# Performance work log

Hardware: AMD Instinct MI355X
Metric: run time of the kernel (lower is better)

The kernel has to match this reference:

```python
import jax, jax.numpy as jnp
import numpy as np

K = 20
EPS = 1e-5


def _lrelu(x):
    return jax.nn.leaky_relu(x, 0.2)


def _bn(x, axes):
    # Training-mode batch norm with default affine (gamma=1, beta=0)
    m = jnp.mean(x, axis=axes, keepdims=True)
    v = jnp.var(x, axis=axes, keepdims=True)
    return (x - m) / jnp.sqrt(v + EPS)


def _get_graph_feature(x, k):
    # x: [B, C, N] -> [B, 2C, N, k]
    xx = jnp.sum(x * x, axis=1)                     # [B, N]
    inner = jnp.einsum('bcn,bcm->bnm', x, x)        # [B, N, N]
    pd = 2.0 * inner - xx[:, :, None] - xx[:, None, :]  # -||xi-xj||^2
    idx = jax.lax.top_k(pd, k)[1]                   # [B, N, k] nearest neighbors
    xt = jnp.transpose(x, (0, 2, 1))                # [B, N, C]
    feat = jax.vmap(lambda a, i: a[i])(xt, idx)     # [B, N, k, C] gathered neighbors
    center = jnp.broadcast_to(xt[:, :, None, :], feat.shape)
    out = jnp.concatenate([feat - center, center], axis=-1)  # [B, N, k, 2C]
    return jnp.transpose(out, (0, 3, 1, 2))


def _pconv(w, x):
    # 1x1 Conv2d, no bias: [O,C] x [B,C,N,k] -> [B,O,N,k]
    return jnp.einsum('oc,bcnk->bonk', w, x)


def _transform_net(x0, t_w1, t_w2, t_w3, t_fc1_w, t_fc2_w, t_fc2_b, t_fc3_w, t_fc3_b):
    h = _lrelu(_bn(_pconv(t_w1, x0), (0, 2, 3)))    # [B,64,N,k]
    h = _lrelu(_bn(_pconv(t_w2, h), (0, 2, 3)))     # [B,128,N,k]
    h = jnp.max(h, axis=-1)                         # [B,128,N]
    h = jnp.einsum('oc,bcn->bon', t_w3, h)          # [B,1024,N]
    h = _lrelu(_bn(h, (0, 2)))
    h = jnp.max(h, axis=-1)                         # [B,1024]
    h = _lrelu(_bn(h @ t_fc1_w.T, (0,)))            # [B,512]
    h = _lrelu(_bn(h @ t_fc2_w.T + t_fc2_b, (0,)))  # [B,256]
    h = h @ t_fc3_w.T + t_fc3_b                     # [B,9]
    h = h + jnp.eye(3, dtype=h.dtype).reshape(1, 9)
    return h.reshape(-1, 3, 3)


def setup_inputs() -> dict:
    key = jax.random.key(0)
    ks = jax.random.split(key, 16)
    s = 0.05
    B, N = 8, 1024
    return {
        'x': jax.random.normal(ks[0], (B, 3, N), jnp.float32),
        't_w1': jax.random.normal(ks[1], (64, 6), jnp.float32) * s,
        't_w2': jax.random.normal(ks[2], (128, 64), jnp.float32) * s,
        't_w3': jax.random.normal(ks[3], (1024, 128), jnp.float32) * s,
        't_fc1_w': jax.random.normal(ks[4], (512, 1024), jnp.float32) * s,
        't_fc2_w': jax.random.normal(ks[5], (256, 512), jnp.float32) * s,
        't_fc2_b': jnp.zeros((256,), jnp.float32),
        't_fc3_w': jax.random.normal(ks[6], (9, 256), jnp.float32) * s,
        't_fc3_b': jnp.zeros((9,), jnp.float32),
        'w1': jax.random.normal(ks[7], (64, 6), jnp.float32) * s,
        'w2': jax.random.normal(ks[8], (64, 128), jnp.float32) * s,
        'w3': jax.random.normal(ks[9], (128, 128), jnp.float32) * s,
        'w4': jax.random.normal(ks[10], (256, 256), jnp.float32) * s,
        'w6': jax.random.normal(ks[11], (1024, 512), jnp.float32) * s,
    }


def reference(x, t_w1, t_w2, t_w3, t_fc1_w, t_fc2_w, t_fc2_b, t_fc3_w, t_fc3_b,
              w1, w2, w3, w4, w6):
    # Input transform
    x0 = _get_graph_feature(x, K)                   # [B,6,N,k]
    T = _transform_net(x0, t_w1, t_w2, t_w3, t_fc1_w, t_fc2_w, t_fc2_b,
                       t_fc3_w, t_fc3_b)            # [B,3,3]
    x = jnp.einsum('bij,bjn->bin', T, x)            # [B,3,N]

    # EdgeConv stack
    g = _get_graph_feature(x, K)
    x1 = jnp.max(_lrelu(_bn(_pconv(w1, g), (0, 2, 3))), axis=-1)   # [B,64,N]
    g = _get_graph_feature(x1, K)
    x2 = jnp.max(_lrelu(_bn(_pconv(w2, g), (0, 2, 3))), axis=-1)   # [B,64,N]
    g = _get_graph_feature(x2, K)
    x3 = jnp.max(_lrelu(_bn(_pconv(w3, g), (0, 2, 3))), axis=-1)   # [B,128,N]
    g = _get_graph_feature(x3, K)
    x4 = jnp.max(_lrelu(_bn(_pconv(w4, g), (0, 2, 3))), axis=-1)   # [B,256,N]

    x_cat = jnp.concatenate([x1, x2, x3, x4], axis=1)              # [B,512,N]
    x_fea = x_cat  # adapt_layer_off: source unavailable, identity passthrough

    h = jnp.einsum('oc,bcn->bon', w6, x_fea)                       # [B,1024,N]
    h = _lrelu(_bn(h, (0, 2)))
    return jnp.max(h, axis=-1)                                     # [B,1024]
```

## Files before the change

kernel.cpp:

```cpp
#include <hip/hip_runtime.h>
#include <math.h>

#define BN_ 8
#define NN 1024
#define KK 20
#define EPSBN 1e-5f
#define FXSCALE 1048576.0f

typedef unsigned long long u64;

__device__ __forceinline__ float lrelu(float x){ return x > 0.f ? x : 0.2f*x; }

__device__ __forceinline__ unsigned fmap(float x){
  unsigned u = __float_as_uint(x);
  return (u & 0x80000000u) ? ~u : (u | 0x80000000u);
}
__device__ __forceinline__ float funmap(unsigned m){
  unsigned u = (m & 0x80000000u) ? (m & 0x7FFFFFFFu) : ~m;
  return __uint_as_float(u);
}

__device__ __forceinline__ void statadd(u64* SP, int O, int ch, int o, float s, float s2){
  atomicAdd(&SP[(size_t)ch*2*O + o],     (u64)(long long)llrintf(s  * FXSCALE));
  atomicAdd(&SP[(size_t)ch*2*O + O + o], (u64)(long long)llrintf(s2 * FXSCALE));
}

__global__ void k_transq(const float* __restrict__ src, long bs, int C,
                         float* __restrict__ xt, float* __restrict__ xx)
{
  int g = blockIdx.x*256 + threadIdx.x;
  if (g >= BN_*NN) return;
  int b = g >> 10, n = g & 1023;
  const float* s = src + (long)b*bs + n;
  float* d = xt + (long)g*C;
  float ss = 0.f;
  for (int c = 0; c < C; ++c){ float v = s[(long)c*NN]; d[c] = v; ss += v*v; }
  xx[g] = ss;
}

__global__ __launch_bounds__(256) void k_knn(
    const float* __restrict__ X, long bsX,
    const float* __restrict__ XT, const float* __restrict__ XX,
    int* __restrict__ IDX, int C)
{
  extern __shared__ float sm[];
  int tid = threadIdx.x;
  int wave = tid >> 6, lane = tid & 63;
  int row0 = blockIdx.x << 2;
  int b = row0 >> 10;
  int i0 = row0 & 1023;
  for (int t = tid; t < 4*C; t += 256){
    int rr = t / C, cc = t - rr*C;
    sm[t] = XT[((long)(b<<10) + i0 + rr)*C + cc];
  }
  __syncthreads();
  const float* xb = X + (long)b*bsX;
  float acc[16];
  #pragma unroll
  for (int q=0;q<16;q++) acc[q]=0.f;
  const float* xi = sm + wave*C;
  for (int c = 0; c < C; ++c){
    const float* xr = xb + (long)c*NN + lane;
    float xiv = xi[c];
    #pragma unroll
    for (int q=0;q<16;q++) acc[q] = fmaf(xiv, xr[q*64], acc[q]);
  }
  const float* xxb = XX + (b<<10);
  float xxj[16];
  #pragma unroll
  for (int q=0;q<16;q++) xxj[q] = xxb[q*64 + lane];
  int row = i0 + wave;
  float xxi = xxb[row];
  #pragma unroll
  for (int q=0;q<16;q++) acc[q] = 2.f*acc[q] - xxi - xxj[q];

  int outbase = ((b<<10) + row)*KK;
  for (int round=0; round<KK; ++round){
    float bv = -INFINITY; int bq = 0;
    #pragma unroll
    for (int q=0;q<16;q++){ float v = acc[q]; if (v > bv){ bv = v; bq = q; } }
    int bj = bq*64 + lane;
    #pragma unroll
    for (int off=32; off>0; off>>=1){
      float ov = __shfl_xor(bv, off);
      int oj = __shfl_xor(bj, off);
      if (ov > bv || (ov == bv && oj < bj)){ bv = ov; bj = oj; }
    }
    bool mine = (lane == (bj & 63));
    int mq = bj >> 6;
    #pragma unroll
    for (int q=0;q<16;q++)
      acc[q] = (mine && q == mq) ? -INFINITY : acc[q];
    if (lane == 0) IDX[outbase + round] = bj;
  }
}

__global__ void k_edgeconv3(const float* __restrict__ XT, const int* __restrict__ IDX,
                            const float* __restrict__ W, float* __restrict__ YMT,
                            u64* __restrict__ SP)
{
  __shared__ float nb[KK*3];
  __shared__ float ctr[3];
  __shared__ int is[KK];
  const int C = 3, O = 64;
  int tid = threadIdx.x;
  int bn = blockIdx.x;
  int b = bn >> 10;
  if (tid < KK) is[tid] = IDX[bn*KK + tid];
  __syncthreads();
  if (tid < 60){ int k = tid/3, c = tid - k*3; nb[tid] = XT[((long)(b<<10)+is[k])*C + c]; }
  if (tid < 3) ctr[tid] = XT[(long)bn*C + tid];
  __syncthreads();
  int o = tid;
  const float* wp = W + (long)o*2*C;
  float yc = 0.f;
  #pragma unroll
  for (int c = 0; c < 3; ++c) yc = fmaf(wp[C+c] - wp[c], ctr[c], yc);
  float acc[KK];
  #pragma unroll
  for (int k=0;k<KK;k++) acc[k] = yc;
  #pragma unroll
  for (int c = 0; c < 3; ++c){
    float wf = wp[c];
    #pragma unroll
    for (int k=0;k<KK;k++) acc[k] = fmaf(wf, nb[k*3+c], acc[k]);
  }
  float mx = -INFINITY, s = 0.f, s2 = 0.f;
  #pragma unroll
  for (int k=0;k<KK;k++){ float v = acc[k]; mx = fmaxf(mx, v); s += v; s2 = fmaf(v,v,s2); }
  YMT[(long)bn*O + o] = mx;
  statadd(SP, O, bn & 63, o, s, s2);
}

template<int C, int O>
__global__ __launch_bounds__(256) void k_gemm_ab(
    const float* __restrict__ XT, const float* __restrict__ WP,
    float* __restrict__ AB)
{
  constexpr int P = 16;
  constexpr int TWO = 2*O;
  constexpr int CO = (TWO + 255)/256;
  __shared__ __align__(16) float Xs[P][C];
  int tid = threadIdx.x;
  long bn0 = (long)blockIdx.x * P;
  for (int t = tid; t < P*C; t += 256) (&Xs[0][0])[t] = XT[bn0*C + t];
  __syncthreads();
  float acc[CO][P];
  #pragma unroll
  for (int j=0;j<CO;j++)
    #pragma unroll
    for (int r=0;r<P;r++) acc[j][r] = 0.f;
  for (int c4 = 0; c4 < C/4; ++c4){
    float4 w[CO];
    #pragma unroll
    for (int j=0;j<CO;j++){
      int o = tid + j*256;
      if (o < TWO) w[j] = *(const float4*)(WP + ((size_t)c4*TWO + o)*4);
    }
    #pragma unroll
    for (int r=0;r<P;r++){
      float4 xv = *(const float4*)(&Xs[r][c4*4]);
      #pragma unroll
      for (int j=0;j<CO;j++){
        acc[j][r] = fmaf(w[j].x, xv.x, acc[j][r]);
        acc[j][r] = fmaf(w[j].y, xv.y, acc[j][r]);
        acc[j][r] = fmaf(w[j].z, xv.z, acc[j][r]);
        acc[j][r] = fmaf(w[j].w, xv.w, acc[j][r]);
      }
    }
  }
  #pragma unroll
  for (int j=0;j<CO;j++){
    int o = tid + j*256;
    if (o < TWO)
      for (int r=0;r<P;r++) AB[(bn0 + r)*TWO + o] = acc[j][r];
  }
}

template<int O, int P>
__global__ __launch_bounds__(256) void k_egather(
    const float* __restrict__ AB, const int* __restrict__ IDX,
    float* __restrict__ YMT, u64* __restrict__ SP)
{
  constexpr int TWO = 2*O;
  constexpr int S = 256/O;
  constexpr int PS = P/S;
  __shared__ int is[P][KK];
  int tid = threadIdx.x;
  long bn0 = (long)blockIdx.x * P;
  long b10 = (bn0 >> 10) << 10;
  for (int t = tid; t < P*KK; t += 256) (&is[0][0])[t] = IDX[bn0*KK + t];
  __syncthreads();
  int strand = tid / O;
  int o = tid - strand*O;
  float s = 0.f, s2 = 0.f;
  #pragma unroll
  for (int ps = 0; ps < PS; ++ps){
    int p = strand*PS + ps;
    long bn = bn0 + p;
    float bv = AB[bn*TWO + O + o];
    float mx = -INFINITY;
    #pragma unroll
    for (int k = 0; k < KK; ++k){
      long row = b10 + is[p][k];
      float v = AB[row*TWO + o] + bv;
      mx = fmaxf(mx, v);
      s += v; s2 = fmaf(v,v,s2);
    }
    YMT[bn*O + o] = mx;
  }
  int ch = ((int)blockIdx.x * S + strand) & 63;
  statadd(SP, O, ch, o, s, s2);
}

__global__ void k_bnfin(const u64* __restrict__ SP, float* __restrict__ MV, int O, float cnt)
{
  int o = blockIdx.x*blockDim.x + threadIdx.x;
  if (o >= O) return;
  long long S = 0, S2 = 0;
  for (int ch = 0; ch < 64; ++ch){
    S  += (long long)SP[(size_t)ch*2*O + o];
    S2 += (long long)SP[(size_t)ch*2*O + O + o];
  }
  double m = (double)S / ((double)FXSCALE * (double)cnt);
  double ms2 = (double)S2 / ((double)FXSCALE * (double)cnt);
  double var = ms2 - m*m;
  MV[o] = (float)m;
  MV[O + o] = (float)(1.0 / sqrt(var + (double)EPSBN));
}

__global__ __launch_bounds__(64) void k_tconv2(
    const float* __restrict__ XT, const int* __restrict__ IDX,
    const float* __restrict__ W1, const float* __restrict__ MV1,
    const float* __restrict__ W2T, float* __restrict__ M2T, u64* __restrict__ SP)
{
  __shared__ float nb[KK*3];
  __shared__ float ctr[3];
  __shared__ __align__(16) float h1t[64*KK];
  __shared__ int is[KK];
  int tid = threadIdx.x;
  int bn = blockIdx.x;
  int b = bn >> 10;
  if (tid < KK) is[tid] = IDX[bn*KK + tid];
  __syncthreads();
  if (tid < 60){ int k = tid/3, c = tid - k*3; nb[tid] = XT[((long)(b<<10)+is[k])*3 + c]; }
  if (tid < 3) ctr[tid] = XT[(long)bn*3 + tid];
  __syncthreads();
  {
    const float* wp = W1 + tid*6;
    float w0=wp[0], w1=wp[1], w2=wp[2];
    float cterm = fmaf(wp[3]-w0, ctr[0], fmaf(wp[4]-w1, ctr[1], (wp[5]-w2)*ctr[2]));
    float m = MV1[tid], iv = MV1[64+tid];
    #pragma unroll
    for (int k=0;k<KK;k++){
      float y = cterm;
      y = fmaf(w0, nb[k*3],   y);
      y = fmaf(w1, nb[k*3+1], y);
      y = fmaf(w2, nb[k*3+2], y);
      h1t[tid*KK + k] = lrelu((y - m) * iv);
    }
  }
  __syncthreads();
  float acc[2][KK];
  #pragma unroll
  for (int j=0;j<2;j++)
    #pragma unroll
    for (int k=0;k<KK;k++) acc[j][k]=0.f;
  #pragma unroll 2
  for (int c=0;c<64;++c){
    float wv0 = W2T[c*128 + tid];
    float wv1 = W2T[c*128 + 64 + tid];
    const float4* hp = (const float4*)(h1t + c*KK);
    float hv[KK];
    #pragma unroll
    for (int q=0;q<5;q++){
      float4 v4 = hp[q];
      hv[q*4]=v4.x; hv[q*4+1]=v4.y; hv[q*4+2]=v4.z; hv[q*4+3]=v4.w;
    }
    #pragma unroll
    for (int k=0;k<KK;k++){
      acc[0][k] = fmaf(wv0, hv[k], acc[0][k]);
      acc[1][k] = fmaf(wv1, hv[k], acc[1][k]);
    }
  }
  int ch = bn & 63;
  #pragma unroll
  for (int j=0;j<2;j++){
    int o = tid + j*64;
    float mx=-INFINITY, s=0.f, s2=0.f;
    #pragma unroll
    for (int k=0;k<KK;k++){ float v = acc[j][k]; mx = fmaxf(mx, v); s += v; s2 = fmaf(v,v,s2); }
    M2T[(long)bn*128 + o] = mx;
    statadd(SP, 128, ch, o, s, s2);
  }
}

__global__ void k_apply_t(const float* __restrict__ SRC, const float* __restrict__ MV,
                          int O, float* __restrict__ DST, long dbs, int choff,
                          float* __restrict__ XTN, float* __restrict__ XXN)
{
  int bn = blockIdx.x*64 + threadIdx.x;
  if (bn >= BN_*NN) return;
  int b = bn >> 10, n = bn & 1023;
  const float4* src = (const float4*)(SRC + (long)bn*O);
  float4* xo = XTN ? (float4*)(XTN + (long)bn*O) : nullptr;
  float ss = 0.f;
  for (int o4 = 0; o4 < O/4; ++o4){
    float4 v = src[o4];
    float vv[4] = {v.x, v.y, v.z, v.w};
    float rr[4];
    #pragma unroll
    for (int u=0;u<4;u++){
      int o = o4*4+u;
      float t = lrelu((vv[u] - MV[o]) * MV[O+o]);
      rr[u] = t;
      ss = fmaf(t,t,ss);
      DST[(long)b*dbs + (long)(choff+o)*NN + n] = t;
    }
    if (xo) xo[o4] = make_float4(rr[0],rr[1],rr[2],rr[3]);
  }
  if (XXN) XXN[bn] = ss;
}

__global__ void k_wprep_t(const float* __restrict__ W, float* __restrict__ WT, int O, int C)
{
  int g = blockIdx.x*256+threadIdx.x;
  if (g >= O*C) return;
  int o = g / C, c = g - o*C;
  WT[(long)c*O + o] = W[g];
}

__global__ void k_wprep_q(const float* __restrict__ W, float* __restrict__ WQ, int C)
{
  int g = blockIdx.x*256+threadIdx.x;
  if (g >= 1024*C) return;
  int o = g / C, c = g - o*C;
  int j = o >> 8, t = o & 255;
  WQ[((size_t)c*256 + t)*4 + j] = W[g];
}

__global__ void k_wprep_e2(const float* __restrict__ W, float* __restrict__ WP, int O, int C)
{
  int g = blockIdx.x*256+threadIdx.x;
  if (g >= O*C) return;
  int o = g / C, c = g - o*C;
  float wf = W[(long)o*2*C + c];
  float wc = W[(long)o*2*C + C + c];
  size_t base = ((size_t)(c>>2)*(2*O))*4 + (c&3);
  WP[base + (size_t)o*4]       = wf;
  WP[base + (size_t)(O+o)*4]   = wc - wf;
}

__global__ __launch_bounds__(256, 1) void k_gemm_sm(
    const float* __restrict__ WQ, const float* __restrict__ X,
    long bsX, int C, unsigned* __restrict__ MX, u64* __restrict__ SP)
{
  int tid = threadIdx.x;
  int bt = blockIdx.x;
  int b = bt >> 6;
  int n0 = (bt & 63) << 4;
  const float* xrow = X + (long)b*bsX + n0;
  float acc[4][16];
  #pragma unroll
  for (int j=0;j<4;j++)
    #pragma unroll
    for (int i=0;i<16;i++) acc[j][i]=0.f;
  const float4* wq = (const float4*)WQ;

  auto gemm_step = [&](int cc, float4 wv){
    const float4* xc = (const float4*)(xrow + (size_t)cc*NN);
    float4 xa = xc[0], xb2 = xc[1], xe = xc[2], xf = xc[3];
    float wj[4] = {wv.x, wv.y, wv.z, wv.w};
    #pragma unroll
    for (int j=0;j<4;j++){
      float ww = wj[j];
      acc[j][0]=fmaf(ww,xa.x,acc[j][0]);  acc[j][1]=fmaf(ww,xa.y,acc[j][1]);
      acc[j][2]=fmaf(ww,xa.z,acc[j][2]);  acc[j][3]=fmaf(ww,xa.w,acc[j][3]);
      acc[j][4]=fmaf(ww,xb2.x,acc[j][4]);  acc[j][5]=fmaf(ww,xb2.y,acc[j][5]);
      acc[j][6]=fmaf(ww,xb2.z,acc[j][6]);  acc[j][7]=fmaf(ww,xb2.w,acc[j][7]);
      acc[j][8]=fmaf(ww,xe.x,acc[j][8]);  acc[j][9]=fmaf(ww,xe.y,acc[j][9]);
      acc[j][10]=fmaf(ww,xe.z,acc[j][10]); acc[j][11]=fmaf(ww,xe.w,acc[j][11]);
      acc[j][12]=fmaf(ww,xf.x,acc[j][12]); acc[j][13]=fmaf(ww,xf.y,acc[j][13]);
      acc[j][14]=fmaf(ww,xf.z,acc[j][14]); acc[j][15]=fmaf(ww,xf.w,acc[j][15]);
    }
  };

  float4 w0 = wq[tid];
  float4 w1 = wq[256 + tid];
  for (int c = 0; c < C-2; c += 2){
    float4 p0 = wq[(size_t)(c+2)*256 + tid];
    float4 p1 = wq[(size_t)(c+3)*256 + tid];
    gemm_step(c,   w0);
    gemm_step(c+1, w1);
    w0 = p0; w1 = p1;
  }
  gemm_step(C-2, w0);
  gemm_step(C-1, w1);

  int ch = bt & 63;
  #pragma unroll
  for (int j=0;j<4;j++){
    int o = tid + j*256;
    float mx=-INFINITY, s=0.f, s2=0.f;
    #pragma unroll
    for (int i=0;i<16;i++){ float v=acc[j][i]; mx=fmaxf(mx,v); s+=v; s2=fmaf(v,v,s2); }
    atomicMax(&MX[(b<<10) + o], fmap(mx));
    statadd(SP, 1024, ch, o, s, s2);
  }
}

__global__ void k_finmax(const unsigned* __restrict__ MX, const float* __restrict__ MV,
                         float* __restrict__ OUT)
{
  int g = blockIdx.x*256+threadIdx.x;
  if (g >= BN_*1024) return;
  int o = g & 1023;
  OUT[g] = lrelu((funmap(MX[g]) - MV[o]) * MV[1024+o]);
}

__global__ __launch_bounds__(256) void k_fcbn(
    const float* __restrict__ A, const float* __restrict__ W,
    const float* __restrict__ bias, int C, int F, float* __restrict__ Z)
{
  int wv = threadIdx.x >> 6, lane = threadIdx.x & 63;
  int f = blockIdx.x*4 + wv;
  if (f >= F) return;
  const float* w = W + (long)f*C;
  float acc[8];
  #pragma unroll
  for (int b=0;b<8;b++) acc[b]=0.f;
  for (int c = lane; c < C; c += 64){
    float wvv = w[c];
    #pragma unroll
    for (int b=0;b<8;b++) acc[b] = fmaf(wvv, A[b*C + c], acc[b]);
  }
  #pragma unroll
  for (int b=0;b<8;b++){
    #pragma unroll
    for (int off=32; off>0; off>>=1) acc[b] += __shfl_xor(acc[b], off);
  }
  float bs = bias ? bias[f] : 0.f;
  float m = 0.f;
  #pragma unroll
  for (int b=0;b<8;b++){ acc[b] += bs; m += acc[b]; }
  m *= 0.125f;
  float var = 0.f;
  #pragma unroll
  for (int b=0;b<8;b++){ float d = acc[b]-m; var = fmaf(d,d,var); }
  var *= 0.125f;
  float is = rsqrtf(var + EPSBN);
  if (lane < 8) Z[lane*F + f] = lrelu((acc[lane]-m)*is);
}

__global__ __launch_bounds__(256) void k_fc3w(
    const float* __restrict__ A, const float* __restrict__ W,
    const float* __restrict__ bias, float* __restrict__ T9)
{
  int g = blockIdx.x*4 + (threadIdx.x >> 6);
  int lane = threadIdx.x & 63;
  if (g >= 72) return;
  int b = g / 9, j = g - b*9;
  const float* a = A + b*256;
  const float* w = W + j*256;
  float s = 0.f;
  for (int c = lane; c < 256; c += 64) s = fmaf(a[c], w[c], s);
  #pragma unroll
  for (int off=32; off>0; off>>=1) s += __shfl_xor(s, off);
  if (lane == 0){
    s += bias[j];
    if (j==0 || j==4 || j==8) s += 1.f;
    T9[g] = s;
  }
}

__global__ void k_tapply(const float* __restrict__ Xin, const float* __restrict__ T9,
                         float* __restrict__ Xtr)
{
  int g = blockIdx.x*256+threadIdx.x;
  if (g >= BN_*3*NN) return;
  int n = g & 1023;
  int i = (g >> 10) % 3;
  int b = g / (3*NN);
  const float* t = T9 + b*9 + i*3;
  const float* xb = Xin + (long)b*3*NN + n;
  Xtr[g] = fmaf(t[0], xb[0], fmaf(t[1], xb[NN], t[2]*xb[2*NN]));
}

extern "C" void kernel_launch(void* const* d_in, const int* in_sizes, int n_in,
                              void* d_out, int out_size, void* d_ws, size_t ws_size,
                              hipStream_t stream)
{
  (void)in_sizes; (void)n_in; (void)out_size;
  const float* x     = (const float*)d_in[0];
  const float* tw1   = (const float*)d_in[1];
  const float* tw2   = (const float*)d_in[2];
  const float* tw3   = (const float*)d_in[3];
  const float* tfc1w = (const float*)d_in[4];
  const float* tfc2w = (const float*)d_in[5];
  const float* tfc2b = (const float*)d_in[6];
  const float* tfc3w = (const float*)d_in[7];
  const float* tfc3b = (const float*)d_in[8];
  const float* w1    = (const float*)d_in[9];
  const float* w2    = (const float*)d_in[10];
  const float* w3    = (const float*)d_in[11];
  const float* w4    = (const float*)d_in[12];
  const float* w6    = (const float*)d_in[13];
  float* out = (float*)d_out;

  char* ws = (char*)d_ws;
  size_t off = 0;
  auto alloc = [&](size_t bytes) -> void* {
    off = (off + 255) & ~(size_t)255;
    void* p = ws + off;
    off += bytes;
    return p;
  };
  auto spb = [](int O){ return (size_t)64*2*O*8; };

  float*    xt   = (float*)alloc((size_t)BN_*NN*128*4);
  float*    xx   = (float*)alloc((size_t)BN_*NN*4);
  int*      idx  = (int*)  alloc((size_t)BN_*NN*KK*4);
  float*    ymt  = (float*)alloc((size_t)BN_*NN*256*4);
  float*    ab   = (float*)alloc((size_t)BN_*NN*512*4);
  float*    xcat = (float*)alloc((size_t)BN_*512*NN*4);
  float*    xtr  = (float*)alloc((size_t)BN_*3*NN*4);
  float*    m2   = (float*)alloc((size_t)BN_*128*NN*4);
  size_t zoff0 = (off + 255) & ~(size_t)255;
  u64*      sp_e1 = (u64*)alloc(spb(64));
  u64*      sp_tc = (u64*)alloc(spb(128));
  u64*      sp_g1 = (u64*)alloc(spb(1024));
  u64*      sp_L1 = (u64*)alloc(spb(64));
  u64*      sp_L2 = (u64*)alloc(spb(64));
  u64*      sp_L3 = (u64*)alloc(spb(128));
  u64*      sp_L4 = (u64*)alloc(spb(256));
  u64*      sp_g2 = (u64*)alloc(spb(1024));
  unsigned* mxu1  = (unsigned*)alloc((size_t)BN_*1024*4);
  unsigned* mxu2  = (unsigned*)alloc((size_t)BN_*1024*4);
  size_t ztotal = off - zoff0;
  float*    mv1  = (float*)alloc(2*64*4);
  float*    mv2  = (float*)alloc(2*128*4);
  float*    mv3  = (float*)alloc(2*1024*4);
  float*    mvL  = (float*)alloc(2*256*4);
  float*    mv6  = (float*)alloc(2*1024*4);
  float*    vbuf = (float*)alloc((size_t)BN_*1024*4);
  float*    z1   = (float*)alloc((size_t)BN_*512*4);
  float*    z2   = (float*)alloc((size_t)BN_*256*4);
  float*    T9   = (float*)alloc(72*4);
  float*    wt3q = (float*)alloc((size_t)128*1024*4);
  float*    w6q  = (float*)alloc((size_t)512*1024*4);
  float*    wt2t = (float*)alloc((size_t)64*128*4);
  float*    w2p  = (float*)alloc((size_t)64*128*4);
  float*    w3p  = (float*)alloc((size_t)64*256*4);
  float*    w4p  = (float*)alloc((size_t)128*512*4);
  if (off > ws_size) return;

  float* m2t = ymt;

  const float CNTK = 8.f*1024.f*20.f;
  const float CNTN = 8.f*1024.f;

  hipMemsetAsync((char*)ws + zoff0, 0, ztotal, stream);

  k_wprep_t<<<(128*64+255)/256, 256, 0, stream>>>(tw2, wt2t, 128, 64);
  k_wprep_q<<<(1024*128)/256, 256, 0, stream>>>(tw3, wt3q, 128);
  k_wprep_q<<<(1024*512)/256, 256, 0, stream>>>(w6, w6q, 512);
  k_wprep_e2<<<(64*64+255)/256, 256, 0, stream>>>(w2, w2p, 64, 64);
  k_wprep_e2<<<(128*64+255)/256, 256, 0, stream>>>(w3, w3p, 128, 64);
  k_wprep_e2<<<(256*128+255)/256, 256, 0, stream>>>(w4, w4p, 256, 128);

  k_transq<<<32, 256, 0, stream>>>(x, 3L*NN, 3, xt, xx);
  k_knn<<<2048, 256, 4*3*4, stream>>>(x, 3L*NN, xt, xx, idx, 3);
  k_edgeconv3<<<BN_*NN, 64, 0, stream>>>(xt, idx, tw1, ymt, sp_e1);
  k_bnfin<<<1, 64, 0, stream>>>(sp_e1, mv1, 64, CNTK);
  k_tconv2<<<BN_*NN, 64, 0, stream>>>(xt, idx, tw1, mv1, wt2t, m2t, sp_tc);
  k_bnfin<<<2, 64, 0, stream>>>(sp_tc, mv2, 128, CNTK);
  k_apply_t<<<128, 64, 0, stream>>>(m2t, mv2, 128, m2, 128L*NN, 0, nullptr, nullptr);
  k_gemm_sm<<<BN_*64, 256, 0, stream>>>(wt3q, m2, 128L*NN, 128, mxu1, sp_g1);
  k_bnfin<<<16, 64, 0, stream>>>(sp_g1, mv3, 1024, CNTN);
  k_finmax<<<32, 256, 0, stream>>>(mxu1, mv3, vbuf);
  k_fcbn<<<128, 256, 0, stream>>>(vbuf, tfc1w, nullptr, 1024, 512, z1);
  k_fcbn<<<64, 256, 0, stream>>>(z1, tfc2w, tfc2b, 512, 256, z2);
  k_fc3w<<<18, 256, 0, stream>>>(z2, tfc3w, tfc3b, T9);
  k_tapply<<<(BN_*3*NN)/256, 256, 0, stream>>>(x, T9, xtr);

  k_transq<<<32, 256, 0, stream>>>(xtr, 3L*NN, 3, xt, xx);
  k_knn<<<2048, 256, 4*3*4, stream>>>(xtr, 3L*NN, xt, xx, idx, 3);
  k_edgeconv3<<<BN_*NN, 64, 0, stream>>>(xt, idx, w1, ymt, sp_L1);
  k_bnfin<<<1, 64, 0, stream>>>(sp_L1, mvL, 64, CNTK);
  k_apply_t<<<128, 64, 0, stream>>>(ymt, mvL, 64, xcat, 512L*NN, 0, xt, xx);
  k_knn<<<2048, 256, 4*64*4, stream>>>(xcat, 512L*NN, xt, xx, idx, 64);
  k_gemm_ab<64,64><<<512, 256, 0, stream>>>(xt, w2p, ab);
  k_egather<64,16><<<512, 256, 0, stream>>>(ab, idx, ymt, sp_L2);
  k_bnfin<<<1, 64, 0, stream>>>(sp_L2, mvL, 64, CNTK);
  k_apply_t<<<128, 64, 0, stream>>>(ymt, mvL, 64, xcat, 512L*NN, 64, xt, xx);
  k_knn<<<2048, 256, 4*64*4, stream>>>(xcat + 64L*NN, 512L*NN, xt, xx, idx, 64);
  k_gemm_ab<64,128><<<512, 256, 0, stream>>>(xt, w3p, ab);
  k_egather<128,16><<<512, 256, 0, stream>>>(ab, idx, ymt, sp_L3);
  k_bnfin<<<2, 64, 0, stream>>>(sp_L3, mvL, 128, CNTK);
  k_apply_t<<<128, 64, 0, stream>>>(ymt, mvL, 128, xcat, 512L*NN, 128, xt, xx);
  k_knn<<<2048, 256, 4*128*4, stream>>>(xcat + 128L*NN, 512L*NN, xt, xx, idx, 128);
  k_gemm_ab<128,256><<<512, 256, 0, stream>>>(xt, w4p, ab);
  k_egather<256,16><<<512, 256, 0, stream>>>(ab, idx, ymt, sp_L4);
  k_bnfin<<<4, 64, 0, stream>>>(sp_L4, mvL, 256, CNTK);
  k_apply_t<<<128, 64, 0, stream>>>(ymt, mvL, 256, xcat, 512L*NN, 256, nullptr, nullptr);

  k_gemm_sm<<<BN_*64, 256, 0, stream>>>(w6q, xcat, 512L*NN, 512, mxu2, sp_g2);
  k_bnfin<<<16, 64, 0, stream>>>(sp_g2, mv6, 1024, CNTN);
  k_finmax<<<32, 256, 0, stream>>>(mxu2, mv6, out);
}
```

Baseline: 976.8 us.

## Use radix-select top-k and two rows per wave in kNN kernel

The kNN kernel now computes two query rows per wave, so each loaded column of candidate points is reused for two rows and the grid is halved. The 20 rounds of argmax with shuffle reductions are replaced by a 32-bit radix select on order-preserving keys, built from ballot/popcount, followed by one compaction pass that writes indices via mbcnt. This is meant to cut shuffle-heavy selection cost and global loads. The output order of neighbors changes (by column position instead of sorted by distance), and the extra accumulators raise register pressure.

```diff
diff --git a/kernel.cpp b/kernel.cpp
--- a/kernel.cpp
+++ b/kernel.cpp
@@ -18,6 +18,11 @@
 __device__ __forceinline__ float funmap(unsigned m){
   unsigned u = (m & 0x80000000u) ? (m & 0x7FFFFFFFu) : ~m;
   return __uint_as_float(u);
+}
+
+__device__ __forceinline__ int mbcnt64(u64 m){
+  return __builtin_amdgcn_mbcnt_hi((unsigned)(m >> 32),
+         __builtin_amdgcn_mbcnt_lo((unsigned)m, 0));
 }
 
 __device__ __forceinline__ void statadd(u64* SP, int O, int ch, int o, float s, float s2){
@@ -46,52 +51,78 @@
   extern __shared__ float sm[];
   int tid = threadIdx.x;
   int wave = tid >> 6, lane = tid & 63;
-  int row0 = blockIdx.x << 2;
-  int b = row0 >> 10;
-  int i0 = row0 & 1023;
-  for (int t = tid; t < 4*C; t += 256){
+  int b = blockIdx.x >> 7;
+  int i0 = (blockIdx.x & 127) << 3;
+  for (int t = tid; t < 8*C; t += 256){
     int rr = t / C, cc = t - rr*C;
     sm[t] = XT[((long)(b<<10) + i0 + rr)*C + cc];
   }
   __syncthreads();
   const float* xb = X + (long)b*bsX;
-  float acc[16];
-  #pragma unroll
-  for (int q=0;q<16;q++) acc[q]=0.f;
-  const float* xi = sm + wave*C;
+  float acc[2][16];
+  #pragma unroll
+  for (int r=0;r<2;r++)
+    #pragma unroll
+    for (int q=0;q<16;q++) acc[r][q]=0.f;
+  const float* xi = sm + (wave*2)*C;
   for (int c = 0; c < C; ++c){
     const float* xr = xb + (long)c*NN + lane;
-    float xiv = xi[c];
-    #pragma unroll
-    for (int q=0;q<16;q++) acc[q] = fmaf(xiv, xr[q*64], acc[q]);
+    float xv[16];
+    #pragma unroll
+    for (int q=0;q<16;q++) xv[q] = xr[q*64];
+    #pragma unroll
+    for (int r=0;r<2;r++){
+      float xiv = xi[r*C + c];
+      #pragma unroll
+      for (int q=0;q<16;q++) acc[r][q] = fmaf(xiv, xv[q], acc[r][q]);
+    }
   }
   const float* xxb = XX + (b<<10);
   float xxj[16];
   #pragma unroll
   for (int q=0;q<16;q++) xxj[q] = xxb[q*64 + lane];
-  int row = i0 + wave;
-  float xxi = xxb[row];
-  #pragma unroll
-  for (int q=0;q<16;q++) acc[q] = 2.f*acc[q] - xxi - xxj[q];
-
-  int outbase = ((b<<10) + row)*KK;
-  for (int round=0; round<KK; ++round){
-    float bv = -INFINITY; int bq = 0;
-    #pragma unroll
-    for (int q=0;q<16;q++){ float v = acc[q]; if (v > bv){ bv = v; bq = q; } }
-    int bj = bq*64 + lane;
-    #pragma unroll
-    for (int off=32; off>0; off>>=1){
-      float ov = __shfl_xor(bv, off);
-      int oj = __shfl_xor(bj, off);
-      if (ov > bv || (ov == bv && oj < bj)){ bv = ov; bj = oj; }
-    }
-    bool mine = (lane == (bj & 63));
-    int mq = bj >> 6;
-    #pragma unroll
-    for (int q=0;q<16;q++)
-      acc[q] = (mine && q == mq) ? -INFINITY : acc[q];
-    if (lane == 0) IDX[outbase + round] = bj;
+  int row0 = i0 + wave*2;
+  #pragma unroll
+  for (int r=0;r<2;r++){
+    float xxi = xxb[row0 + r];
+    #pragma unroll
+    for (int q=0;q<16;q++) acc[r][q] = 2.f*acc[r][q] - xxi - xxj[q];
+  }
+
+  for (int r=0;r<2;r++){
+    unsigned u[16];
+    #pragma unroll
+    for (int q=0;q<16;q++) u[q] = fmap(acc[r][q]);
+    unsigned P = 0;
+    for (int bit = 31; bit >= 0; --bit){
+      unsigned cand = P | (1u << bit);
+      int c = 0;
+      #pragma unroll
+      for (int q=0;q<16;q++) c += (int)__popcll(__ballot(u[q] >= cand));
+      if (c >= KK) P = cand;
+    }
+    int nG = 0;
+    #pragma unroll
+    for (int q=0;q<16;q++) nG += (int)__popcll(__ballot(u[q] > P));
+    int navail = KK - nG;
+    int slot = 0;
+    int outb = ((b<<10) + row0 + r)*KK;
+    #pragma unroll
+    for (int q=0;q<16;q++){
+      u64 mg = __ballot(u[q] > P);
+      u64 me = __ballot(u[q] == P);
+      int cg = (int)__popcll(mg);
+      int ce = (int)__popcll(me);
+      int take_e = navail < ce ? navail : ce;
+      if (u[q] > P){
+        IDX[outb + slot + mbcnt64(mg)] = q*64 + lane;
+      } else if (u[q] == P){
+        int rk = mbcnt64(me);
+        if (rk < take_e) IDX[outb + slot + cg + rk] = q*64 + lane;
+      }
+      slot += cg + take_e;
+      navail -= take_e;
+    }
   }
 }
 
@@ -569,7 +600,7 @@
   k_wprep_e2<<<(256*128+255)/256, 256, 0, stream>>>(w4, w4p, 256, 128);
 
   k_transq<<<32, 256, 0, stream>>>(x, 3L*NN, 3, xt, xx);
-  k_knn<<<2048, 256, 4*3*4, stream>>>(x, 3L*NN, xt, xx, idx, 3);
+  k_knn<<<1024, 256, 8*3*4, stream>>>(x, 3L*NN, xt, xx, idx, 3);
   k_edgeconv3<<<BN_*NN, 64, 0, stream>>>(xt, idx, tw1, ymt, sp_e1);
   k_bnfin<<<1, 64, 0, stream>>>(sp_e1, mv1, 64, CNTK);
   k_tconv2<<<BN_*NN, 64, 0, stream>>>(xt, idx, tw1, mv1, wt2t, m2t, sp_tc);
@@ -584,21 +615,21 @@
   k_tapply<<<(BN_*3*NN)/256, 256, 0, stream>>>(x, T9, xtr);
 
   k_transq<<<32, 256, 0, stream>>>(xtr, 3L*NN, 3, xt, xx);
-  k_knn<<<2048, 256, 4*3*4, stream>>>(xtr, 3L*NN, xt, xx, idx, 3);
+  k_knn<<<1024, 256, 8*3*4, stream>>>(xtr, 3L*NN, xt, xx, idx, 3);
   k_edgeconv3<<<BN_*NN, 64, 0, stream>>>(xt, idx, w1, ymt, sp_L1);
   k_bnfin<<<1, 64, 0, stream>>>(sp_L1, mvL, 64, CNTK);
   k_apply_t<<<128, 64, 0, stream>>>(ymt, mvL, 64, xcat, 512L*NN, 0, xt, xx);
-  k_knn<<<2048, 256, 4*64*4, stream>>>(xcat, 512L*NN, xt, xx, idx, 64);
+  k_knn<<<1024, 256, 8*64*4, stream>>>(xcat, 512L*NN, xt, xx, idx, 64);
   k_gemm_ab<64,64><<<512, 256, 0, stream>>>(xt, w2p, ab);
   k_egather<64,16><<<512, 256, 0, stream>>>(ab, idx, ymt, sp_L2);
   k_bnfin<<<1, 64, 0, stream>>>(sp_L2, mvL, 64, CNTK);
   k_apply_t<<<128, 64, 0, stream>>>(ymt, mvL, 64, xcat, 512L*NN, 64, xt, xx);
-  k_knn<<<2048, 256, 4*64*4, stream>>>(xcat + 64L*NN, 512L*NN, xt, xx, idx, 64);
+  k_knn<<<1024, 256, 8*64*4, stream>>>(xcat + 64L*NN, 512L*NN, xt, xx, idx, 64);
   k_gemm_ab<64,128><<<512, 256, 0, stream>>>(xt, w3p, ab);
   k_egather<128,16><<<512, 256, 0, stream>>>(ab, idx, ymt, sp_L3);
   k_bnfin<<<2, 64, 0, stream>>>(sp_L3, mvL, 128, CNTK);
   k_apply_t<<<128, 64, 0, stream>>>(ymt, mvL, 128, xcat, 512L*NN, 128, xt, xx);
-  k_knn<<<2048, 256, 4*128*4, stream>>>(xcat + 128L*NN, 512L*NN, xt, xx, idx, 128);
+  k_knn<<<1024, 256, 8*128*4, stream>>>(xcat + 128L*NN, 512L*NN, xt, xx, idx, 128);
   k_gemm_ab<128,256><<<512, 256, 0, stream>>>(xt, w4p, ab);
   k_egather<256,16><<<512, 256, 0, stream>>>(ab, idx, ymt, sp_L4);
   k_bnfin<<<4, 64, 0, stream>>>(sp_L4, mvL, 256, CNTK);
```

Result: faster. 847.7 us (-13.2%).
